# Performance work log

Measured on AMD Instinct MI355X. Metric: run time of the kernel, lower is better.

The kernel has to match this reference:

```python
import jax, jax.numpy as jnp
import numpy as np

B, M, W, C, NN, J, ED, EMB = 8, 4096, 128, 32, 16, 4, 5, 2
EPS = 1e-5


def setup_inputs() -> dict:
    key = jax.random.key(0)
    ks = jax.random.split(key, 30)
    s = 0.05
    x = jax.random.normal(ks[0], (B, M, W), jnp.float32)
    pseudo = jax.random.normal(ks[1], (M * NN, EMB), jnp.float32)
    # structured indices: row r scatters its NN attention weights into row r of the m x m matrix
    nbr = jax.random.randint(ks[2], (M, NN), 0, M)
    L_idx = (jnp.arange(M)[:, None] * M + nbr).reshape(-1).astype(jnp.int32)
    inp = dict(x=x, pseudo=pseudo, L_idx=L_idx)
    inp['edge_w'] = jax.random.normal(ks[3], (ED, EMB), jnp.float32) * s
    inp['edge_b'] = jnp.zeros((ED,), jnp.float32)
    # Gaussian mixture params per layer (J components, encode_dim each); reset_parameters -> N(0,1)
    inp['mu0'] = jax.random.normal(ks[4], (J, ED), jnp.float32)
    inp['sigma0'] = jax.random.normal(ks[5], (J, ED), jnp.float32)
    inp['mu1'] = jax.random.normal(ks[6], (J, ED), jnp.float32)
    inp['sigma1'] = jax.random.normal(ks[7], (J, ED), jnp.float32)
    # layer 0: W -> C ; layer 1: C -> C
    inp['l1w0'] = jax.random.normal(ks[8], (C, W), jnp.float32) * s
    inp['l1b0'] = jnp.zeros((C,), jnp.float32)
    inp['l2w0'] = jax.random.normal(ks[9], (C, W), jnp.float32) * s
    inp['l2b0'] = jnp.zeros((C,), jnp.float32)
    inp['l1w1'] = jax.random.normal(ks[10], (C, C), jnp.float32) * s
    inp['l1b1'] = jnp.zeros((C,), jnp.float32)
    inp['l2w1'] = jax.random.normal(ks[11], (C, C), jnp.float32) * s
    inp['l2b1'] = jnp.zeros((C,), jnp.float32)
    inp['bn_g0'] = jnp.ones((C,), jnp.float32)
    inp['bn_b0'] = jnp.zeros((C,), jnp.float32)
    inp['bn_g1'] = jnp.ones((C,), jnp.float32)
    inp['bn_b1'] = jnp.zeros((C,), jnp.float32)
    inp['fc1w'] = jax.random.normal(ks[12], (256, M * C), jnp.float32) * 0.005
    inp['fc1b'] = jnp.zeros((256,), jnp.float32)
    inp['fc2w'] = jax.random.normal(ks[13], (53, 256), jnp.float32) * s
    inp['fc2b'] = jnp.zeros((53,), jnp.float32)
    return inp


def _get_L(pseudo, L_idx, edge_w, edge_b, mu, sigma, dtype):
    # Gaussian-mixture edge attention: u^T diag(sigma) u per component, summed, exp(-0.5 *)
    emb = pseudo @ edge_w.T + edge_b                      # (E, ED), E = M*NN
    u = emb[None, :, :] - mu[:, None, :]                  # (J, E, ED)
    q = jnp.sum(u * u * sigma[:, None, :], axis=-1)       # (J, E)
    w = jnp.sum(jnp.exp(-0.5 * q), axis=0)                # (E,)
    attn = jax.nn.softmax(w.reshape(M, NN), axis=1).reshape(-1)
    return jnp.zeros(M * M, dtype).at[L_idx].set(attn).reshape(M, M)


def _layer(x, L, w1, b1, w2, b2, g, bb):
    Lx = jnp.einsum('mn,bnf->bmf', L, x)                  # graph conv
    h = Lx @ w1.T + b1 + x @ w2.T + b2                    # (B, M, C)
    # BatchNorm1d (training mode): stats over batch and node dims, biased variance
    mean = jnp.mean(h, axis=(0, 1))
    var = jnp.var(h, axis=(0, 1))
    h = (h - mean) * jax.lax.rsqrt(var + EPS) * g + bb
    return jax.nn.relu(h)


def reference(x, pseudo, L_idx, edge_w, edge_b, mu0, sigma0, mu1, sigma1,
              l1w0, l1b0, l2w0, l2b0, l1w1, l1b1, l2w1, l2b1,
              bn_g0, bn_b0, bn_g1, bn_b1, fc1w, fc1b, fc2w, fc2b):
    L0 = _get_L(pseudo, L_idx, edge_w, edge_b, mu0, sigma0, x.dtype)
    h = _layer(x, L0, l1w0, l1b0, l2w0, l2b0, bn_g0, bn_b0)
    L1 = _get_L(pseudo, L_idx, edge_w, edge_b, mu1, sigma1, x.dtype)
    h = _layer(h, L1, l1w1, l1b1, l2w1, l2b1, bn_g1, bn_b1)
    flat = h.reshape(B, M * C)
    out = jax.nn.relu(flat @ fc1w.T + fc1b)               # dropout = identity (eval)
    return out @ fc2w.T + fc2b                            # (B, 53)
```

## Files before the change

kernel.cpp:

```cpp
#include <hip/hip_runtime.h>

#define B_ 8
#define M_ 4096
#define W_ 128
#define C_ 32
#define NN_ 16

typedef short s16x8 __attribute__((ext_vector_type(8)));
typedef float f32x4 __attribute__((ext_vector_type(4)));

static __device__ __forceinline__ unsigned short f2bf(float f) {
  unsigned u = __builtin_bit_cast(unsigned, f);
  u = u + 0x7FFFu + ((u >> 16) & 1u);
  return (unsigned short)(u >> 16);
}
static __device__ __forceinline__ s16x8 cvt8v(float4 a, float4 b) {
  s16x8 r;
  r[0] = (short)f2bf(a.x); r[1] = (short)f2bf(a.y);
  r[2] = (short)f2bf(a.z); r[3] = (short)f2bf(a.w);
  r[4] = (short)f2bf(b.x); r[5] = (short)f2bf(b.y);
  r[6] = (short)f2bf(b.z); r[7] = (short)f2bf(b.w);
  return r;
}
static __device__ __forceinline__ float safeexp(float a) {
  return expf(fminf(a, 87.f));
}

__global__ void poison_kernel(float* __restrict__ out, int n, float val) {
  int t = blockIdx.x * blockDim.x + threadIdx.x;
  if (t < n) out[t] = val;
}

__global__ __launch_bounds__(256) void init_kernel(
    float* __restrict__ fc1acc, const float* __restrict__ fc1b,
    float* __restrict__ bn) {
  int g = blockIdx.x * 256 + threadIdx.x;
  if (g < 2048) fc1acc[g] = fc1b[g & 255];
  else if (g < 34816) bn[g - 2048] = 0.f;
}

__global__ __launch_bounds__(256) void attn_kernel(
    const float* __restrict__ pseudo, const int* __restrict__ Lidx,
    const float* __restrict__ edge_w, const float* __restrict__ edge_b,
    const float* __restrict__ mu0, const float* __restrict__ sg0,
    const float* __restrict__ mu1, const float* __restrict__ sg1,
    float* __restrict__ we0, float* __restrict__ we1, int* __restrict__ colb) {
  int m = blockIdx.x * 256 + threadIdx.x;
  if (m >= M_) return;
  float w0[NN_], w1[NN_];
  int col[NN_];
#pragma unroll
  for (int n = 0; n < NN_; n++) {
    int e = m * NN_ + n;
    float p0 = pseudo[e * 2], p1 = pseudo[e * 2 + 1];
    float emb[5];
#pragma unroll
    for (int d = 0; d < 5; d++)
      emb[d] = p0 * edge_w[d * 2] + p1 * edge_w[d * 2 + 1] + edge_b[d];
    float a0 = 0.f, a1 = 0.f;
#pragma unroll
    for (int j = 0; j < 4; j++) {
      float qa = 0.f, qb = 0.f;
#pragma unroll
      for (int d = 0; d < 5; d++) {
        float u0 = emb[d] - mu0[j * 5 + d];
        qa += u0 * u0 * sg0[j * 5 + d];
        float u1 = emb[d] - mu1[j * 5 + d];
        qb += u1 * u1 * sg1[j * 5 + d];
      }
      a0 += safeexp(-0.5f * qa);
      a1 += safeexp(-0.5f * qb);
    }
    w0[n] = a0; w1[n] = a1;
    col[n] = Lidx[e] % M_;
  }
  float mx0 = w0[0], mx1 = w1[0];
#pragma unroll
  for (int n = 1; n < NN_; n++) { mx0 = fmaxf(mx0, w0[n]); mx1 = fmaxf(mx1, w1[n]); }
  float s0 = 0.f, s1 = 0.f;
#pragma unroll
  for (int n = 0; n < NN_; n++) {
    w0[n] = safeexp(w0[n] - mx0); s0 += w0[n];
    w1[n] = safeexp(w1[n] - mx1); s1 += w1[n];
  }
  float r0 = 1.f / s0, r1 = 1.f / s1;
#pragma unroll
  for (int n = 0; n < NN_; n++) {
    bool last = true;
#pragma unroll
    for (int n2 = n + 1; n2 < NN_; n2++)
      if (col[n2] == col[n]) last = false;
    int e = m * NN_ + n;
    we0[e] = last ? w0[n] * r0 : 0.f;
    we1[e] = last ? w1[n] * r1 : 0.f;
    colb[e] = col[n];
  }
}

__global__ __launch_bounds__(256) void proj0_kernel(
    const float* __restrict__ x, const float* __restrict__ l1w0,
    const float* __restrict__ l2w0, float* __restrict__ G) {
  int lane = threadIdx.x & 63, wave = threadIdx.x >> 6;
  int l16 = lane & 15, quad = lane >> 4;
  int tile = blockIdx.x * 4 + wave;
  s16x8 bf[4][4];
#pragma unroll
  for (int kit = 0; kit < 4; kit++) {
#pragma unroll
    for (int ct = 0; ct < 4; ct++) {
      int out = ct * 16 + l16;
      const float* src = (out < 32 ? l1w0 + out * 128 : l2w0 + (out - 32) * 128)
                         + kit * 32 + quad * 8;
      bf[kit][ct] = cvt8v(*(const float4*)src, *(const float4*)(src + 4));
    }
  }
  f32x4 acc[4];
#pragma unroll
  for (int ct = 0; ct < 4; ct++) acc[ct] = (f32x4){0.f, 0.f, 0.f, 0.f};
  int row = tile * 16 + l16;
  const float* xr = x + (size_t)row * 128 + quad * 8;
#pragma unroll
  for (int kit = 0; kit < 4; kit++) {
    const float* ap = xr + kit * 32;
    s16x8 a = cvt8v(*(const float4*)ap, *(const float4*)(ap + 4));
#pragma unroll
    for (int ct = 0; ct < 4; ct++)
      acc[ct] = __builtin_amdgcn_mfma_f32_16x16x32_bf16(a, bf[kit][ct], acc[ct], 0, 0, 0);
  }
  int rbase = tile * 16 + quad * 4;
#pragma unroll
  for (int ct = 0; ct < 4; ct++)
#pragma unroll
    for (int i = 0; i < 4; i++)
      G[(size_t)(rbase + i) * 64 + ct * 16 + l16] = acc[ct][i];
}

__global__ __launch_bounds__(256) void conv_kernel(
    const float* __restrict__ G,
    const float* __restrict__ we, const int* __restrict__ colb,
    const float* __restrict__ b1c, const float* __restrict__ b2c,
    float* __restrict__ h, float* __restrict__ bns, float* __restrict__ bnq) {
  __shared__ float s_we[8][16];
  __shared__ int   s_cn[8][16];
  __shared__ float s_s[32], s_q[32];
  int tid = threadIdx.x;
  if (tid < 128) {
    int row = tid >> 4, nn = tid & 15;
    int m = (blockIdx.x * 8 + row) & 4095;
    s_we[row][nn] = we[m * 16 + nn];
    s_cn[row][nn] = colb[m * 16 + nn];
  } else if (tid < 160) {
    s_s[tid - 128] = 0.f;
    s_q[tid - 128] = 0.f;
  }
  __syncthreads();
  int row = tid >> 5, c = tid & 31;
  int r = blockIdx.x * 8 + row;
  int b = r >> 12;
  const float* Gb = G + ((size_t)b << 18);
  float acc = 0.f;
#pragma unroll
  for (int nn = 0; nn < NN_; nn++)
    acc += s_we[row][nn] * Gb[s_cn[row][nn] * 64 + c];
  float hv = acc + G[(size_t)r * 64 + 32 + c] + b1c[c] + b2c[c];
  h[(size_t)r * 32 + c] = hv;
  atomicAdd(&s_s[c], hv);
  atomicAdd(&s_q[c], hv * hv);
  __syncthreads();
  if (tid < 32) {
    int slot = blockIdx.x & 255;
    atomicAdd(&bns[tid * 256 + slot], s_s[tid]);
    atomicAdd(&bnq[tid * 256 + slot], s_q[tid]);
  }
}

__global__ __launch_bounds__(256) void bnfin_kernel(
    const float* __restrict__ bns, const float* __restrict__ bnq,
    const float* __restrict__ g, const float* __restrict__ bb,
    float* __restrict__ scale, float* __restrict__ shift) {
  __shared__ float red[2][8][32];
  int tid = threadIdx.x;
  int c = tid & 31, part = tid >> 5;
  float s = 0.f, q = 0.f;
#pragma unroll 8
  for (int i = 0; i < 32; i++) {
    s += bns[c * 256 + part * 32 + i];
    q += bnq[c * 256 + part * 32 + i];
  }
  red[0][part][c] = s;
  red[1][part][c] = q;
  __syncthreads();
  if (tid < 32) {
    float S = 0.f, Q = 0.f;
#pragma unroll
    for (int p = 0; p < 8; p++) { S += red[0][p][tid]; Q += red[1][p][tid]; }
    float mean = S * (1.f / 32768.f);
    float var = fmaxf(Q * (1.f / 32768.f) - mean * mean, 0.f);
    float sc = g[tid] * rsqrtf(var + 1e-5f);
    scale[tid] = sc;
    shift[tid] = bb[tid] - mean * sc;
  }
}

__global__ __launch_bounds__(256) void proj1_kernel(
    const float* __restrict__ h0, const float* __restrict__ sc0,
    const float* __restrict__ l1w1, const float* __restrict__ l2w1,
    float* __restrict__ G) {
  int lane = threadIdx.x & 63, wave = threadIdx.x >> 6;
  int l16 = lane & 15, quad = lane >> 4;
  int tile = blockIdx.x * 4 + wave;
  s16x8 bf[4];
#pragma unroll
  for (int ct = 0; ct < 4; ct++) {
    int out = ct * 16 + l16;
    const float* src = (out < 32 ? l1w1 + out * 32 : l2w1 + (out - 32) * 32) + quad * 8;
    bf[ct] = cvt8v(*(const float4*)src, *(const float4*)(src + 4));
  }
  float scv[8], shv[8];
#pragma unroll
  for (int j = 0; j < 8; j++) {
    scv[j] = sc0[quad * 8 + j];
    shv[j] = sc0[32 + quad * 8 + j];
  }
  int row = tile * 16 + l16;
  const float* hr = h0 + (size_t)row * 32 + quad * 8;
  float4 hv0 = *(const float4*)hr;
  float4 hv1 = *(const float4*)(hr + 4);
  float av[8] = {hv0.x, hv0.y, hv0.z, hv0.w, hv1.x, hv1.y, hv1.z, hv1.w};
  s16x8 a;
#pragma unroll
  for (int j = 0; j < 8; j++)
    a[j] = (short)f2bf(fmaxf(av[j] * scv[j] + shv[j], 0.f));
  f32x4 acc[4];
#pragma unroll
  for (int ct = 0; ct < 4; ct++) {
    f32x4 z = {0.f, 0.f, 0.f, 0.f};
    acc[ct] = __builtin_amdgcn_mfma_f32_16x16x32_bf16(a, bf[ct], z, 0, 0, 0);
  }
  int rbase = tile * 16 + quad * 4;
#pragma unroll
  for (int ct = 0; ct < 4; ct++)
#pragma unroll
    for (int i = 0; i < 4; i++)
      G[(size_t)(rbase + i) * 64 + ct * 16 + l16] = acc[ct][i];
}

__global__ __launch_bounds__(256) void fc1_kernel(
    const float* __restrict__ h1, const float* __restrict__ sc1,
    const float* __restrict__ fc1w, float* __restrict__ fc1acc) {
  __shared__ short als[16 * 1024];
  int tid = threadIdx.x;
  int kc = blockIdx.x >> 2;
  int og = blockIdx.x & 3;
  size_t kbase = (size_t)kc << 10;
  for (int s = tid; s < 4096; s += 256) {
    int rowb = s >> 8;
    int k4 = (s & 255) << 2;
    short4 v4 = {0, 0, 0, 0};
    if (rowb < 8) {
      float4 hv = *(const float4*)(h1 + ((size_t)rowb << 17) + kbase + k4);
      int c = k4 & 31;
      float4 scv = *(const float4*)(sc1 + c);
      float4 shv = *(const float4*)(sc1 + 32 + c);
      v4.x = (short)f2bf(fmaxf(hv.x * scv.x + shv.x, 0.f));
      v4.y = (short)f2bf(fmaxf(hv.y * scv.y + shv.y, 0.f));
      v4.z = (short)f2bf(fmaxf(hv.z * scv.z + shv.z, 0.f));
      v4.w = (short)f2bf(fmaxf(hv.w * scv.w + shv.w, 0.f));
    }
    int byte = ((rowb << 11) + (k4 << 1)) ^ ((rowb & 7) << 4);
    *(short4*)((char*)als + byte) = v4;
  }
  __syncthreads();
  int lane = tid & 63, wave = tid >> 6;
  int l16 = lane & 15, quad = lane >> 4;
  const float* wrow = fc1w + (size_t)(og * 64 + wave * 16 + l16) * 131072
                      + kbase + quad * 8;
  int abase = (l16 << 11) + (quad << 4);
  int axor = (l16 & 7) << 4;
  f32x4 acc = {0.f, 0.f, 0.f, 0.f};
#pragma unroll 4
  for (int kk = 0; kk < 32; kk++) {
    const float* wp = wrow + kk * 32;
    s16x8 bfr = cvt8v(*(const float4*)wp, *(const float4*)(wp + 4));
    s16x8 afr = *(const s16x8*)((const char*)als + ((abase + (kk << 6)) ^ axor));
    acc = __builtin_amdgcn_mfma_f32_16x16x32_bf16(afr, bfr, acc, 0, 0, 0);
  }
  if (quad < 2) {
    int o = og * 64 + wave * 16 + l16;
#pragma unroll
    for (int i = 0; i < 4; i++)
      atomicAdd(&fc1acc[(quad * 4 + i) * 256 + o], acc[i]);
  }
}

__global__ void fc2_kernel(const float* __restrict__ fc1acc,
                           const float* __restrict__ fc2w,
                           const float* __restrict__ fc2b,
                           float* __restrict__ out) {
  int t = blockIdx.x * blockDim.x + threadIdx.x;
  if (t >= 424) return;
  int b = t / 53, j = t - b * 53;
  float s = fc2b[j];
  const float* fa = fc1acc + b * 256;
  const float* wr = fc2w + j * 256;
#pragma unroll 8
  for (int o = 0; o < 256; o++) s += fmaxf(fa[o], 0.f) * wr[o];
  out[t] = s;
}

extern "C" void kernel_launch(void* const* d_in, const int* in_sizes, int n_in,
                              void* d_out, int out_size, void* d_ws, size_t ws_size,
                              hipStream_t stream) {
  float* out = (float*)d_out;
  int bad = 0;
  if (n_in != 25) bad = 2;
  else if (in_sizes[0] != 4194304) bad = 3;
  else if (in_sizes[2] != 65536) bad = 4;
  else if (in_sizes[21] != 33554432) bad = 5;
  else if (out_size != 424) bad = 6;
  else if (ws_size < 13509120) bad = 1;
  if (bad) {
    poison_kernel<<<2, 256, 0, stream>>>(out, out_size, (float)bad * 1.0e6f);
    return;
  }

  const float* x      = (const float*)d_in[0];
  const float* pseudo = (const float*)d_in[1];
  const int*   Lidx   = (const int*)d_in[2];
  const float* edge_w = (const float*)d_in[3];
  const float* edge_b = (const float*)d_in[4];
  const float* mu0    = (const float*)d_in[5];
  const float* sg0    = (const float*)d_in[6];
  const float* mu1    = (const float*)d_in[7];
  const float* sg1    = (const float*)d_in[8];
  const float* l1w0   = (const float*)d_in[9];
  const float* l1b0   = (const float*)d_in[10];
  const float* l2w0   = (const float*)d_in[11];
  const float* l2b0   = (const float*)d_in[12];
  const float* l1w1   = (const float*)d_in[13];
  const float* l1b1   = (const float*)d_in[14];
  const float* l2w1   = (const float*)d_in[15];
  const float* l2b1   = (const float*)d_in[16];
  const float* bng0   = (const float*)d_in[17];
  const float* bnb0   = (const float*)d_in[18];
  const float* bng1   = (const float*)d_in[19];
  const float* bnb1   = (const float*)d_in[20];
  const float* fc1w   = (const float*)d_in[21];
  const float* fc1b   = (const float*)d_in[22];
  const float* fc2w   = (const float*)d_in[23];
  const float* fc2b   = (const float*)d_in[24];

  char* Wp = (char*)d_ws;
  int*   colb   = (int*)  (Wp + 0);
  float* we0    = (float*)(Wp + 262144);
  float* we1    = (float*)(Wp + 524288);
  float* G      = (float*)(Wp + 786432);
  float* h0     = (float*)(Wp + 9175040);
  float* h1     = (float*)(Wp + 9175040);
  float* bn     = (float*)(Wp + 13369344);
  float* sc     = (float*)(Wp + 13500416);
  float* fc1acc = (float*)(Wp + 13500928);

  init_kernel<<<136, 256, 0, stream>>>(fc1acc, fc1b, bn);
  attn_kernel<<<16, 256, 0, stream>>>(pseudo, Lidx, edge_w, edge_b,
                                      mu0, sg0, mu1, sg1, we0, we1, colb);
  proj0_kernel<<<512, 256, 0, stream>>>(x, l1w0, l2w0, G);
  conv_kernel<<<4096, 256, 0, stream>>>(G, we0, colb, l1b0, l2b0,
                                        h0, bn, bn + 8192);
  bnfin_kernel<<<1, 256, 0, stream>>>(bn, bn + 8192, bng0, bnb0, sc, sc + 32);
  proj1_kernel<<<512, 256, 0, stream>>>(h0, sc, l1w1, l2w1, G);
  conv_kernel<<<4096, 256, 0, stream>>>(G, we1, colb, l1b1, l2b1,
                                        h1, bn + 16384, bn + 24576);
  bnfin_kernel<<<1, 256, 0, stream>>>(bn + 16384, bn + 24576, bng1, bnb1,
                                      sc + 64, sc + 96);
  fc1_kernel<<<512, 256, 0, stream>>>(h1, sc + 64, fc1w, fc1acc);
  fc2_kernel<<<2, 256, 0, stream>>>(fc1acc, fc2w, fc2b, out);
}
```

Measured before the change: 346.5 us.

## Fuse all stages into one cooperative persistent kernel with fc1 weight prefetch

Replaces the chain of ten kernel launches with a single cooperative kernel of 1024 blocks that separates stages with grid.sync(). Blocks that are idle during the projection, conv and batchnorm stages stream quarters of the large fc1 weight matrix to warm the cache before fc1 runs. fc1 is split into twice as many smaller K-chunks to match the 1024-block grid, and the projection kernels now load weights inside the MFMA loop instead of holding them in registers, to fit 4 blocks per CU. The risks are grid-sync overhead, and the prefetch only helps if the 128 MB of weights stays resident in cache until fc1 runs; the old multi-kernel path is kept as a fallback.

After: 340.6 us. Within noise of the previous version (-1.7%).

```diff
diff --git a/kernel.cpp b/kernel.cpp
--- a/kernel.cpp
+++ b/kernel.cpp
@@ -1,4 +1,7 @@
 #include <hip/hip_runtime.h>
+#include <hip/hip_cooperative_groups.h>
+
+namespace cg = cooperative_groups;
 
 #define B_ 8
 #define M_ 4096
@@ -31,22 +34,13 @@
   if (t < n) out[t] = val;
 }
 
-__global__ __launch_bounds__(256) void init_kernel(
-    float* __restrict__ fc1acc, const float* __restrict__ fc1b,
-    float* __restrict__ bn) {
-  int g = blockIdx.x * 256 + threadIdx.x;
-  if (g < 2048) fc1acc[g] = fc1b[g & 255];
-  else if (g < 34816) bn[g - 2048] = 0.f;
-}
-
-__global__ __launch_bounds__(256) void attn_kernel(
-    const float* __restrict__ pseudo, const int* __restrict__ Lidx,
+
+static __device__ void attn_row(
+    int m, const float* __restrict__ pseudo, const int* __restrict__ Lidx,
     const float* __restrict__ edge_w, const float* __restrict__ edge_b,
     const float* __restrict__ mu0, const float* __restrict__ sg0,
     const float* __restrict__ mu1, const float* __restrict__ sg1,
     float* __restrict__ we0, float* __restrict__ we1, int* __restrict__ colb) {
-  int m = blockIdx.x * 256 + threadIdx.x;
-  if (m >= M_) return;
   float w0[NN_], w1[NN_];
   int col[NN_];
 #pragma unroll
@@ -97,35 +91,30 @@
   }
 }
 
-__global__ __launch_bounds__(256) void proj0_kernel(
-    const float* __restrict__ x, const float* __restrict__ l1w0,
+static __device__ void proj0_tile(
+    int blk, int tid, const float* __restrict__ x, const float* __restrict__ l1w0,
     const float* __restrict__ l2w0, float* __restrict__ G) {
-  int lane = threadIdx.x & 63, wave = threadIdx.x >> 6;
+  int lane = tid & 63, wave = tid >> 6;
   int l16 = lane & 15, quad = lane >> 4;
-  int tile = blockIdx.x * 4 + wave;
-  s16x8 bf[4][4];
-#pragma unroll
-  for (int kit = 0; kit < 4; kit++) {
-#pragma unroll
-    for (int ct = 0; ct < 4; ct++) {
-      int out = ct * 16 + l16;
-      const float* src = (out < 32 ? l1w0 + out * 128 : l2w0 + (out - 32) * 128)
-                         + kit * 32 + quad * 8;
-      bf[kit][ct] = cvt8v(*(const float4*)src, *(const float4*)(src + 4));
-    }
-  }
+  int tile = blk * 4 + wave;
   f32x4 acc[4];
 #pragma unroll
   for (int ct = 0; ct < 4; ct++) acc[ct] = (f32x4){0.f, 0.f, 0.f, 0.f};
   int row = tile * 16 + l16;
   const float* xr = x + (size_t)row * 128 + quad * 8;
+  int out0 = l16;
 #pragma unroll
   for (int kit = 0; kit < 4; kit++) {
     const float* ap = xr + kit * 32;
     s16x8 a = cvt8v(*(const float4*)ap, *(const float4*)(ap + 4));
 #pragma unroll
-    for (int ct = 0; ct < 4; ct++)
-      acc[ct] = __builtin_amdgcn_mfma_f32_16x16x32_bf16(a, bf[kit][ct], acc[ct], 0, 0, 0);
+    for (int ct = 0; ct < 4; ct++) {
+      int out = ct * 16 + out0;
+      const float* src = (out < 32 ? l1w0 + out * 128 : l2w0 + (out - 32) * 128)
+                         + kit * 32 + quad * 8;
+      s16x8 bf = cvt8v(*(const float4*)src, *(const float4*)(src + 4));
+      acc[ct] = __builtin_amdgcn_mfma_f32_16x16x32_bf16(a, bf, acc[ct], 0, 0, 0);
+    }
   }
   int rbase = tile * 16 + quad * 4;
 #pragma unroll
@@ -135,18 +124,19 @@
       G[(size_t)(rbase + i) * 64 + ct * 16 + l16] = acc[ct][i];
 }
 
-__global__ __launch_bounds__(256) void conv_kernel(
-    const float* __restrict__ G,
-    const float* __restrict__ we, const int* __restrict__ colb,
-    const float* __restrict__ b1c, const float* __restrict__ b2c,
-    float* __restrict__ h, float* __restrict__ bns, float* __restrict__ bnq) {
-  __shared__ float s_we[8][16];
-  __shared__ int   s_cn[8][16];
-  __shared__ float s_s[32], s_q[32];
-  int tid = threadIdx.x;
+static __device__ void conv_block(
+    int cb, int tid, char* smem,
+    const float* __restrict__ G, const float* __restrict__ we,
+    const int* __restrict__ colb, const float* __restrict__ b1c,
+    const float* __restrict__ b2c, float* __restrict__ h,
+    float* __restrict__ bns, float* __restrict__ bnq) {
+  float (*s_we)[16] = (float(*)[16])smem;
+  int   (*s_cn)[16] = (int(*)[16])(smem + 512);
+  float* s_s = (float*)(smem + 1024);
+  float* s_q = (float*)(smem + 1152);
   if (tid < 128) {
     int row = tid >> 4, nn = tid & 15;
-    int m = (blockIdx.x * 8 + row) & 4095;
+    int m = (cb * 8 + row) & 4095;
     s_we[row][nn] = we[m * 16 + nn];
     s_cn[row][nn] = colb[m * 16 + nn];
   } else if (tid < 160) {
@@ -155,7 +145,7 @@
   }
   __syncthreads();
   int row = tid >> 5, c = tid & 31;
-  int r = blockIdx.x * 8 + row;
+  int r = cb * 8 + row;
   int b = r >> 12;
   const float* Gb = G + ((size_t)b << 18);
   float acc = 0.f;
@@ -168,18 +158,17 @@
   atomicAdd(&s_q[c], hv * hv);
   __syncthreads();
   if (tid < 32) {
-    int slot = blockIdx.x & 255;
+    int slot = cb & 255;
     atomicAdd(&bns[tid * 256 + slot], s_s[tid]);
     atomicAdd(&bnq[tid * 256 + slot], s_q[tid]);
   }
 }
 
-__global__ __launch_bounds__(256) void bnfin_kernel(
-    const float* __restrict__ bns, const float* __restrict__ bnq,
+static __device__ void bnfin_block(
+    int tid, char* smem, const float* __restrict__ bns, const float* __restrict__ bnq,
     const float* __restrict__ g, const float* __restrict__ bb,
     float* __restrict__ scale, float* __restrict__ shift) {
-  __shared__ float red[2][8][32];
-  int tid = threadIdx.x;
+  float (*red)[8][32] = (float(*)[8][32])smem;
   int c = tid & 31, part = tid >> 5;
   float s = 0.f, q = 0.f;
 #pragma unroll 8
@@ -202,26 +191,13 @@
   }
 }
 
-__global__ __launch_bounds__(256) void proj1_kernel(
-    const float* __restrict__ h0, const float* __restrict__ sc0,
+static __device__ void proj1_tile(
+    int blk, int tid, const float* __restrict__ h0, const float* __restrict__ sc0,
     const float* __restrict__ l1w1, const float* __restrict__ l2w1,
     float* __restrict__ G) {
-  int lane = threadIdx.x & 63, wave = threadIdx.x >> 6;
+  int lane = tid & 63, wave = tid >> 6;
   int l16 = lane & 15, quad = lane >> 4;
-  int tile = blockIdx.x * 4 + wave;
-  s16x8 bf[4];
-#pragma unroll
-  for (int ct = 0; ct < 4; ct++) {
-    int out = ct * 16 + l16;
-    const float* src = (out < 32 ? l1w1 + out * 32 : l2w1 + (out - 32) * 32) + quad * 8;
-    bf[ct] = cvt8v(*(const float4*)src, *(const float4*)(src + 4));
-  }
-  float scv[8], shv[8];
-#pragma unroll
-  for (int j = 0; j < 8; j++) {
-    scv[j] = sc0[quad * 8 + j];
-    shv[j] = sc0[32 + quad * 8 + j];
-  }
+  int tile = blk * 4 + wave;
   int row = tile * 16 + l16;
   const float* hr = h0 + (size_t)row * 32 + quad * 8;
   float4 hv0 = *(const float4*)hr;
@@ -229,13 +205,19 @@
   float av[8] = {hv0.x, hv0.y, hv0.z, hv0.w, hv1.x, hv1.y, hv1.z, hv1.w};
   s16x8 a;
 #pragma unroll
-  for (int j = 0; j < 8; j++)
-    a[j] = (short)f2bf(fmaxf(av[j] * scv[j] + shv[j], 0.f));
+  for (int j = 0; j < 8; j++) {
+    float scv = sc0[quad * 8 + j];
+    float shv = sc0[32 + quad * 8 + j];
+    a[j] = (short)f2bf(fmaxf(av[j] * scv + shv, 0.f));
+  }
   f32x4 acc[4];
 #pragma unroll
   for (int ct = 0; ct < 4; ct++) {
+    int out = ct * 16 + l16;
+    const float* src = (out < 32 ? l1w1 + out * 32 : l2w1 + (out - 32) * 32) + quad * 8;
+    s16x8 bf = cvt8v(*(const float4*)src, *(const float4*)(src + 4));
     f32x4 z = {0.f, 0.f, 0.f, 0.f};
-    acc[ct] = __builtin_amdgcn_mfma_f32_16x16x32_bf16(a, bf[ct], z, 0, 0, 0);
+    acc[ct] = __builtin_amdgcn_mfma_f32_16x16x32_bf16(a, bf, z, 0, 0, 0);
   }
   int rbase = tile * 16 + quad * 4;
 #pragma unroll
@@ -245,17 +227,17 @@
       G[(size_t)(rbase + i) * 64 + ct * 16 + l16] = acc[ct][i];
 }
 
-__global__ __launch_bounds__(256) void fc1_kernel(
-    const float* __restrict__ h1, const float* __restrict__ sc1,
-    const float* __restrict__ fc1w, float* __restrict__ fc1acc) {
-  __shared__ short als[16 * 1024];
-  int tid = threadIdx.x;
-  int kc = blockIdx.x >> 2;
-  int og = blockIdx.x & 3;
-  size_t kbase = (size_t)kc << 10;
-  for (int s = tid; s < 4096; s += 256) {
-    int rowb = s >> 8;
-    int k4 = (s & 255) << 2;
+static __device__ void fc1_block(
+    int u, int tid, char* smem, const float* __restrict__ h1,
+    const float* __restrict__ sc1, const float* __restrict__ fc1w,
+    float* __restrict__ fc1acc) {
+  short* als = (short*)smem;
+  int kc = u >> 2;
+  int og = u & 3;
+  size_t kbase = (size_t)kc << 9;
+  for (int s = tid; s < 2048; s += 256) {
+    int rowb = s >> 7;
+    int k4 = (s & 127) << 2;
     short4 v4 = {0, 0, 0, 0};
     if (rowb < 8) {
       float4 hv = *(const float4*)(h1 + ((size_t)rowb << 17) + kbase + k4);
@@ -267,38 +249,35 @@
       v4.z = (short)f2bf(fmaxf(hv.z * scv.z + shv.z, 0.f));
       v4.w = (short)f2bf(fmaxf(hv.w * scv.w + shv.w, 0.f));
     }
-    int byte = ((rowb << 11) + (k4 << 1)) ^ ((rowb & 7) << 4);
+    int byte = ((rowb << 10) + (k4 << 1)) ^ ((rowb & 7) << 4);
     *(short4*)((char*)als + byte) = v4;
   }
   __syncthreads();
   int lane = tid & 63, wave = tid >> 6;
   int l16 = lane & 15, quad = lane >> 4;
-  const float* wrow = fc1w + (size_t)(og * 64 + wave * 16 + l16) * 131072
-                      + kbase + quad * 8;
-  int abase = (l16 << 11) + (quad << 4);
+  int o = og * 64 + wave * 16 + l16;
+  const float* wr = fc1w + (size_t)o * 131072 + kbase + quad * 8;
+  int abase = (l16 << 10) + (quad << 4);
   int axor = (l16 & 7) << 4;
   f32x4 acc = {0.f, 0.f, 0.f, 0.f};
 #pragma unroll 4
-  for (int kk = 0; kk < 32; kk++) {
-    const float* wp = wrow + kk * 32;
+  for (int kk = 0; kk < 16; kk++) {
+    const float* wp = wr + kk * 32;
     s16x8 bfr = cvt8v(*(const float4*)wp, *(const float4*)(wp + 4));
     s16x8 afr = *(const s16x8*)((const char*)als + ((abase + (kk << 6)) ^ axor));
     acc = __builtin_amdgcn_mfma_f32_16x16x32_bf16(afr, bfr, acc, 0, 0, 0);
   }
   if (quad < 2) {
-    int o = og * 64 + wave * 16 + l16;
 #pragma unroll
     for (int i = 0; i < 4; i++)
       atomicAdd(&fc1acc[(quad * 4 + i) * 256 + o], acc[i]);
   }
-}
-
-__global__ void fc2_kernel(const float* __restrict__ fc1acc,
-                           const float* __restrict__ fc2w,
-                           const float* __restrict__ fc2b,
-                           float* __restrict__ out) {
-  int t = blockIdx.x * blockDim.x + threadIdx.x;
-  if (t >= 424) return;
+  __syncthreads();
+}
+
+static __device__ void fc2_elem(
+    int t, const float* __restrict__ fc1acc, const float* __restrict__ fc2w,
+    const float* __restrict__ fc2b, float* __restrict__ out) {
   int b = t / 53, j = t - b * 53;
   float s = fc2b[j];
   const float* fa = fc1acc + b * 256;
@@ -306,6 +285,147 @@
 #pragma unroll 8
   for (int o = 0; o < 256; o++) s += fmaxf(fa[o], 0.f) * wr[o];
   out[t] = s;
+}
+
+static __device__ __forceinline__ void prefetch_q(
+    const float* __restrict__ fc1w, int quarter, int idx, int stride) {
+  const float4* p = (const float4*)fc1w + (size_t)quarter * 2097152;
+  float acc = 0.f;
+  for (int i = idx; i < 2097152; i += stride) {
+    float4 v = p[i];
+    acc += v.x + v.y + v.z + v.w;
+  }
+  asm volatile("" :: "v"(acc));
+}
+
+__global__ __launch_bounds__(256, 4) void fused_kernel(
+    const float* __restrict__ x, const float* __restrict__ pseudo,
+    const int* __restrict__ Lidx,
+    const float* __restrict__ edge_w, const float* __restrict__ edge_b,
+    const float* __restrict__ mu0, const float* __restrict__ sg0,
+    const float* __restrict__ mu1, const float* __restrict__ sg1,
+    const float* __restrict__ l1w0, const float* __restrict__ l1b0,
+    const float* __restrict__ l2w0, const float* __restrict__ l2b0,
+    const float* __restrict__ l1w1, const float* __restrict__ l1b1,
+    const float* __restrict__ l2w1, const float* __restrict__ l2b1,
+    const float* __restrict__ bng0, const float* __restrict__ bnb0,
+    const float* __restrict__ bng1, const float* __restrict__ bnb1,
+    const float* __restrict__ fc1w, const float* __restrict__ fc1b,
+    const float* __restrict__ fc2w, const float* __restrict__ fc2b,
+    float* __restrict__ out,
+    int* __restrict__ colb, float* __restrict__ we0, float* __restrict__ we1,
+    float* __restrict__ G, float* __restrict__ h,
+    float* __restrict__ bn, float* __restrict__ sc, float* __restrict__ fc1acc) {
+  __shared__ char smem[16384];
+  cg::grid_group grid = cg::this_grid();
+  int bid = blockIdx.x, tid = threadIdx.x;
+  int gtid = bid * 256 + tid;
+
+  if (gtid < 2048) fc1acc[gtid] = fc1b[gtid & 255];
+  else if (gtid < 34816) bn[gtid - 2048] = 0.f;
+  if (bid < 16)
+    attn_row(gtid, pseudo, Lidx, edge_w, edge_b, mu0, sg0, mu1, sg1, we0, we1, colb);
+  grid.sync();
+
+  if (bid < 512) proj0_tile(bid, tid, x, l1w0, l2w0, G);
+  else           prefetch_q(fc1w, 0, (bid - 512) * 256 + tid, 131072);
+  grid.sync();
+
+  for (int it = 0; it < 4; it++) {
+    __syncthreads();
+    conv_block(bid + it * 1024, tid, smem, G, we0, colb, l1b0, l2b0,
+               h, bn, bn + 8192);
+  }
+  prefetch_q(fc1w, 1, gtid, 262144);
+  grid.sync();
+
+  if (bid == 0) bnfin_block(tid, smem, bn, bn + 8192, bng0, bnb0, sc, sc + 32);
+  else          prefetch_q(fc1w, 2, gtid - 256, 261888);
+  grid.sync();
+
+  if (bid < 512) proj1_tile(bid, tid, h, sc, l1w1, l2w1, G);
+  else           prefetch_q(fc1w, 3, (bid - 512) * 256 + tid, 131072);
+  grid.sync();
+
+  for (int it = 0; it < 4; it++) {
+    __syncthreads();
+    conv_block(bid + it * 1024, tid, smem, G, we1, colb, l1b1, l2b1,
+               h, bn + 16384, bn + 24576);
+  }
+  grid.sync();
+
+  if (bid == 0) bnfin_block(tid, smem, bn + 16384, bn + 24576, bng1, bnb1,
+                            sc + 64, sc + 96);
+  grid.sync();
+
+  fc1_block(bid, tid, smem, h, sc + 64, fc1w, fc1acc);
+  grid.sync();
+
+  if (gtid < 424) fc2_elem(gtid, fc1acc, fc2w, fc2b, out);
+}
+
+__global__ __launch_bounds__(256) void init_kernel(
+    float* __restrict__ fc1acc, const float* __restrict__ fc1b,
+    float* __restrict__ bn) {
+  int g = blockIdx.x * 256 + threadIdx.x;
+  if (g < 2048) fc1acc[g] = fc1b[g & 255];
+  else if (g < 34816) bn[g - 2048] = 0.f;
+}
+
+__global__ __launch_bounds__(256) void attn_kernel(
+    const float* __restrict__ pseudo, const int* __restrict__ Lidx,
+    const float* __restrict__ edge_w, const float* __restrict__ edge_b,
+    const float* __restrict__ mu0, const float* __restrict__ sg0,
+    const float* __restrict__ mu1, const float* __restrict__ sg1,
+    float* __restrict__ we0, float* __restrict__ we1, int* __restrict__ colb) {
+  int m = blockIdx.x * 256 + threadIdx.x;
+  if (m < M_)
+    attn_row(m, pseudo, Lidx, edge_w, edge_b, mu0, sg0, mu1, sg1, we0, we1, colb);
+}
+
+__global__ __launch_bounds__(256) void proj0_kernel(
+    const float* __restrict__ x, const float* __restrict__ l1w0,
+    const float* __restrict__ l2w0, float* __restrict__ G) {
+  proj0_tile(blockIdx.x, threadIdx.x, x, l1w0, l2w0, G);
+}
+
+__global__ __launch_bounds__(256) void conv_kernel(
+    const float* __restrict__ G,
+    const float* __restrict__ we, const int* __restrict__ colb,
+    const float* __restrict__ b1c, const float* __restrict__ b2c,
+    float* __restrict__ h, float* __restrict__ bns, float* __restrict__ bnq) {
+  __shared__ char smem[1280];
+  conv_block(blockIdx.x, threadIdx.x, smem, G, we, colb, b1c, b2c, h, bns, bnq);
+}
+
+__global__ __launch_bounds__(256) void bnfin_kernel(
+    const float* __restrict__ bns, const float* __restrict__ bnq,
+    const float* __restrict__ g, const float* __restrict__ bb,
+    float* __restrict__ scale, float* __restrict__ shift) {
+  __shared__ char smem[2048];
+  bnfin_block(threadIdx.x, smem, bns, bnq, g, bb, scale, shift);
+}
+
+__global__ __launch_bounds__(256) void proj1_kernel(
+    const float* __restrict__ h0, const float* __restrict__ sc0,
+    const float* __restrict__ l1w1, const float* __restrict__ l2w1,
+    float* __restrict__ G) {
+  proj1_tile(blockIdx.x, threadIdx.x, h0, sc0, l1w1, l2w1, G);
+}
+
+__global__ __launch_bounds__(256) void fc1_kernel(
+    const float* __restrict__ h1, const float* __restrict__ sc1,
+    const float* __restrict__ fc1w, float* __restrict__ fc1acc) {
+  __shared__ char smem[16384];
+  fc1_block(blockIdx.x, threadIdx.x, smem, h1, sc1, fc1w, fc1acc);
+}
+
+__global__ void fc2_kernel(const float* __restrict__ fc1acc,
+                           const float* __restrict__ fc2w,
+                           const float* __restrict__ fc2b,
+                           float* __restrict__ out) {
+  int t = blockIdx.x * blockDim.x + threadIdx.x;
+  if (t < 424) fc2_elem(t, fc1acc, fc2w, fc2b, out);
 }
 
 extern "C" void kernel_launch(void* const* d_in, const int* in_sizes, int n_in,
@@ -356,23 +476,42 @@
   float* we1    = (float*)(Wp + 524288);
   float* G      = (float*)(Wp + 786432);
   float* h0     = (float*)(Wp + 9175040);
-  float* h1     = (float*)(Wp + 9175040);
   float* bn     = (float*)(Wp + 13369344);
   float* sc     = (float*)(Wp + 13500416);
   float* fc1acc = (float*)(Wp + 13500928);
 
-  init_kernel<<<136, 256, 0, stream>>>(fc1acc, fc1b, bn);
-  attn_kernel<<<16, 256, 0, stream>>>(pseudo, Lidx, edge_w, edge_b,
-                                      mu0, sg0, mu1, sg1, we0, we1, colb);
-  proj0_kernel<<<512, 256, 0, stream>>>(x, l1w0, l2w0, G);
-  conv_kernel<<<4096, 256, 0, stream>>>(G, we0, colb, l1b0, l2b0,
-                                        h0, bn, bn + 8192);
-  bnfin_kernel<<<1, 256, 0, stream>>>(bn, bn + 8192, bng0, bnb0, sc, sc + 32);
-  proj1_kernel<<<512, 256, 0, stream>>>(h0, sc, l1w1, l2w1, G);
-  conv_kernel<<<4096, 256, 0, stream>>>(G, we1, colb, l1b1, l2b1,
-                                        h1, bn + 16384, bn + 24576);
-  bnfin_kernel<<<1, 256, 0, stream>>>(bn + 16384, bn + 24576, bng1, bnb1,
-                                      sc + 64, sc + 96);
-  fc1_kernel<<<512, 256, 0, stream>>>(h1, sc + 64, fc1w, fc1acc);
-  fc2_kernel<<<2, 256, 0, stream>>>(fc1acc, fc2w, fc2b, out);
-}
+  int maxb = 0;
+  hipError_t oe = hipOccupancyMaxActiveBlocksPerMultiprocessor(&maxb, fused_kernel, 256, 0);
+  bool coop = (oe == hipSuccess && maxb >= 4);
+  if (coop) {
+    void* args[] = {
+      (void*)&x, (void*)&pseudo, (void*)&Lidx, (void*)&edge_w, (void*)&edge_b,
+      (void*)&mu0, (void*)&sg0, (void*)&mu1, (void*)&sg1,
+      (void*)&l1w0, (void*)&l1b0, (void*)&l2w0, (void*)&l2b0,
+      (void*)&l1w1, (void*)&l1b1, (void*)&l2w1, (void*)&l2b1,
+      (void*)&bng0, (void*)&bnb0, (void*)&bng1, (void*)&bnb1,
+      (void*)&fc1w, (void*)&fc1b, (void*)&fc2w, (void*)&fc2b,
+      (void*)&out,
+      (void*)&colb, (void*)&we0, (void*)&we1, (void*)&G, (void*)&h0,
+      (void*)&bn, (void*)&sc, (void*)&fc1acc };
+    hipError_t le = hipLaunchCooperativeKernel((const void*)fused_kernel,
+                                               dim3(1024), dim3(256), args, 0, stream);
+    if (le != hipSuccess) coop = false;
+  }
+  if (!coop) {
+    init_kernel<<<136, 256, 0, stream>>>(fc1acc, fc1b, bn);
+    attn_kernel<<<16, 256, 0, stream>>>(pseudo, Lidx, edge_w, edge_b,
+                                        mu0, sg0, mu1, sg1, we0, we1, colb);
+    proj0_kernel<<<512, 256, 0, stream>>>(x, l1w0, l2w0, G);
+    conv_kernel<<<4096, 256, 0, stream>>>(G, we0, colb, l1b0, l2b0,
+                                          h0, bn, bn + 8192);
+    bnfin_kernel<<<1, 256, 0, stream>>>(bn, bn + 8192, bng0, bnb0, sc, sc + 32);
+    proj1_kernel<<<512, 256, 0, stream>>>(h0, sc, l1w1, l2w1, G);
+    conv_kernel<<<4096, 256, 0, stream>>>(G, we1, colb, l1b1, l2b1,
+                                          h0, bn + 16384, bn + 24576);
+    bnfin_kernel<<<1, 256, 0, stream>>>(bn + 16384, bn + 24576, bng1, bnb1,
+                                        sc + 64, sc + 96);
+    fc1_kernel<<<1024, 256, 0, stream>>>(h0, sc + 64, fc1w, fc1acc);
+    fc2_kernel<<<2, 256, 0, stream>>>(fc1acc, fc2w, fc2b, out);
+  }
+}
```
